# Kernel tuning notes

Measured on AMD Instinct MI355X. Metric: run time of the kernel, lower is better.

## Reference

```python
import jax, jax.numpy as jnp
import numpy as np

D = 384        # residual_depth
QK = 48        # D // qk_dim_div(=8)
E = 768        # D * expand_factor(=2)
NB = 8         # num_blocks
VOCAB = 100
LN_EPS = 1e-5


def _ln(x, g, b):
    m = x.mean(-1, keepdims=True)
    v = x.var(-1, keepdims=True)  # biased, matches torch LayerNorm
    return (x - m) / jnp.sqrt(v + LN_EPS) * g + b


def setup_inputs() -> dict:
    key = jax.random.key(0)
    ks = jax.random.split(key, 5)
    B, S = 4, 2048
    q = jax.random.randint(ks[0], (B, S), 0, 100, dtype=jnp.int32)
    freqs = jnp.exp(jnp.arange(0, D, 2, dtype=jnp.float32) * (-np.log(10000.0) / D))
    # fused expand: rows = qk + qk + expand + expand = 1632
    exp_w = (0.5 / np.sqrt(D) / 2.0) * jax.random.normal(ks[1], (NB, 2 * QK + 2 * E, D), dtype=jnp.float32)
    proj_w = (1.0 / np.sqrt(D) / 2.0 / NB) * jax.random.normal(ks[2], (NB, D, E), dtype=jnp.float32)
    blk_g = jnp.ones((NB, D), jnp.float32)
    blk_b = jnp.zeros((NB, D), jnp.float32)
    ln_g = jnp.ones((D,), jnp.float32)
    ln_b = jnp.zeros((D,), jnp.float32)
    out_w = 0.02 * jax.random.normal(ks[3], (VOCAB, D), dtype=jnp.float32)
    return dict(q=q, freqs=freqs, exp_w=exp_w, proj_w=proj_w,
                blk_g=blk_g, blk_b=blk_b, ln_g=ln_g, ln_b=ln_b, out_w=out_w)


def reference(q, freqs, exp_w, proj_w, blk_g, blk_b, ln_g, ln_b, out_w):
    S = q.shape[1]
    # sinusoidal encoding of integer tokens -> [B,S,D]
    qe = q.astype(jnp.float32)[..., None] * freqs
    x = jnp.concatenate([jnp.sin(qe), jnp.cos(qe)], axis=-1)
    x = _ln(x, ln_g, ln_b)
    # causal mask; position_bias_base is zeros in the source
    bias = jnp.where(jnp.tril(jnp.ones((S, S), bool)), 0.0, -jnp.inf).astype(jnp.float32)
    inv_sqrt_qk = 1.0 / np.sqrt(QK)

    def block(x, p):
        ew, pw, g, b = p
        xn = _ln(x, g, b)
        h = xn @ ew.T                                   # [B,S,1632]
        qh, kh, lin, pg = jnp.split(h, [QK, 2 * QK, 2 * QK + E], axis=-1)
        geglu = lin * jax.nn.gelu(pg, approximate=False)  # [B,S,E]
        loc, val = geglu[..., :E - D], geglu[..., E - D:]  # [B,S,D],[B,S,D]
        sc = jnp.einsum('bqd,bkd->bqk', qh, kh) * inv_sqrt_qk + bias
        attn = jax.nn.softmax(sc, axis=-1) @ val          # [B,S,D]
        out = jnp.concatenate([loc, attn], axis=-1) @ pw.T
        return x + out, None

    x, _ = jax.lax.scan(block, x, (exp_w, proj_w, blk_g, blk_b))
    x = _ln(x, ln_g, ln_b)
    return x @ out_w.T
```

## Files before the change

### kernel.cpp

```cpp
#include <hip/hip_runtime.h>
#include <hip/hip_bf16.h>

#define TOK 8192
#define DM 384
#define QKD 48
#define EM 768
#define NBLK 8
#define NVOCAB 100
#define SEQ 2048
#define HN 1664
#define HNV 1632
#define CH 8
#define NUNITS 2304

using short4v = __attribute__((ext_vector_type(4))) short;
using short8 = __attribute__((ext_vector_type(8))) short;
using f32x4  = __attribute__((ext_vector_type(4))) float;

static __device__ __forceinline__ float bf2f(short s) {
    union { unsigned u; float f; } c; c.u = ((unsigned)(unsigned short)s) << 16; return c.f;
}
static __device__ __forceinline__ short f2bf(float f) {
    union { float f; unsigned u; } c; c.f = f;
    unsigned r = (c.u + 0x7FFFu + ((c.u >> 16) & 1u)) >> 16;
    return (short)r;
}
static __device__ __forceinline__ void gload_lds16(const short* g, short* l) {
    __builtin_amdgcn_global_load_lds((const __attribute__((address_space(1))) void*)g,
                                     (__attribute__((address_space(3))) void*)l, 16, 0, 0);
}

__global__ void k_cvt_all(const float* __restrict__ expw, const float* __restrict__ projw,
                          const float* __restrict__ outw, short* __restrict__ ewb,
                          short* __restrict__ pwb, short* __restrict__ owb) {
    const int n1 = NBLK * HN * DM;
    for (int i = blockIdx.x * 256 + threadIdx.x; i < n1; i += gridDim.x * 256) {
        int L = i / (HN * DM); int rem = i % (HN * DM);
        int r = rem / DM; int c = rem % DM;
        float v = (r < HNV) ? expw[((size_t)L * HNV + r) * DM + c] : 0.f;
        ewb[i] = f2bf(v);
    }
    const int n2 = NBLK * DM * EM;
    for (int i = blockIdx.x * 256 + threadIdx.x; i < n2; i += gridDim.x * 256)
        pwb[i] = f2bf(projw[i]);
    const int n3 = 128 * DM;
    for (int i = blockIdx.x * 256 + threadIdx.x; i < n3; i += gridDim.x * 256) {
        int r = i / DM, c = i % DM;
        owb[i] = f2bf(r < NVOCAB ? outw[r * DM + c] : 0.f);
    }
}

__global__ __launch_bounds__(256) void k_embed(const int* __restrict__ q,
        const float* __restrict__ freqs, const float* __restrict__ lng,
        const float* __restrict__ lnb, float* __restrict__ x) {
    int wid = blockIdx.x * 4 + (threadIdx.x >> 6);
    int lane = threadIdx.x & 63;
    if (wid >= TOK) return;
    float qv = (float)q[wid];
    float v[6]; float s = 0.f, s2 = 0.f;
    #pragma unroll
    for (int i = 0; i < 6; ++i) {
        int d = lane + 64 * i;
        float val;
        if (d < 192) val = sinf(qv * freqs[d]);
        else         val = cosf(qv * freqs[d - 192]);
        v[i] = val; s += val; s2 += val * val;
    }
    #pragma unroll
    for (int m = 1; m < 64; m <<= 1) { s += __shfl_xor(s, m); s2 += __shfl_xor(s2, m); }
    float mean = s * (1.f / DM);
    float var = s2 * (1.f / DM) - mean * mean;
    float rstd = rsqrtf(var + 1e-5f);
    float* xr = x + (size_t)wid * DM;
    #pragma unroll
    for (int i = 0; i < 6; ++i) {
        int d = lane + 64 * i;
        xr[d] = (v[i] - mean) * rstd * lng[d] + lnb[d];
    }
}

__global__ __launch_bounds__(256) void k_ln(const float* __restrict__ x,
        const float* __restrict__ g, const float* __restrict__ b,
        short* __restrict__ xn) {
    int wid = blockIdx.x * 4 + (threadIdx.x >> 6);
    int lane = threadIdx.x & 63;
    if (wid >= TOK) return;
    const float* xr = x + (size_t)wid * DM;
    float v[6]; float s = 0.f, s2 = 0.f;
    #pragma unroll
    for (int i = 0; i < 6; ++i) {
        v[i] = xr[lane + 64 * i]; s += v[i]; s2 += v[i] * v[i];
    }
    #pragma unroll
    for (int m = 1; m < 64; m <<= 1) { s += __shfl_xor(s, m); s2 += __shfl_xor(s2, m); }
    float mean = s * (1.f / DM);
    float var = s2 * (1.f / DM) - mean * mean;
    float rstd = rsqrtf(var + 1e-5f);
    short* xo = xn + (size_t)wid * DM;
    #pragma unroll
    for (int i = 0; i < 6; ++i) {
        int d = lane + 64 * i;
        xo[d] = f2bf((v[i] - mean) * rstd * g[d] + b[d]);
    }
}

__global__ __launch_bounds__(256) void k_gemmh(const short* __restrict__ A,
        const short* __restrict__ Bw, short* __restrict__ cat,
        short* __restrict__ vT, short* __restrict__ qhb, short* __restrict__ khb) {
    __shared__ __align__(16) short As[128 * 32];
    __shared__ __align__(16) short Bs[128 * 32];
    int m0 = blockIdx.x * 128;
    int y = blockIdx.y;
    int t = threadIdx.x;
    int wid = t >> 6, lane = t & 63;
    int wm = (wid >> 1) * 64, wn = (wid & 1) * 64;
    int lr = lane & 15, lg = lane >> 4;
    int seg0 = wid * 2, seg1 = wid * 2 + 1;
    int row0 = seg0 * 16 + (lane >> 2), row1 = seg1 * 16 + (lane >> 2);
    int cu0 = (lane & 3) ^ ((row0 + (row0 >> 2)) & 3);
    int cu1 = (lane & 3) ^ ((row1 + (row1 >> 2)) & 3);
    int brow0, brow1;
    if (y < 12) {
        int s0h = row0 >> 4, s1h = row1 >> 4;
        brow0 = 96 + (s0h & 1) * 768 + y * 64 + (s0h >> 1) * 16 + (row0 & 15);
        brow1 = 96 + (s1h & 1) * 768 + y * 64 + (s1h >> 1) * 16 + (row1 & 15);
    } else {
        brow0 = (row0 < 96) ? row0 : 1632 + (row0 - 96);
        brow1 = (row1 < 96) ? row1 : 1632 + (row1 - 96);
    }
    const short* srcA0 = A + (size_t)(m0 + row0) * DM + cu0 * 8;
    const short* srcA1 = A + (size_t)(m0 + row1) * DM + cu1 * 8;
    const short* srcB0 = Bw + (size_t)brow0 * DM + cu0 * 8;
    const short* srcB1 = Bw + (size_t)brow1 * DM + cu1 * 8;
    short* dA0 = As + seg0 * 512; short* dA1 = As + seg1 * 512;
    short* dB0 = Bs + seg0 * 512; short* dB1 = Bs + seg1 * 512;
    const f32x4 vz = {0.f, 0.f, 0.f, 0.f};
    f32x4 acc[4][4];
    #pragma unroll
    for (int i = 0; i < 4; ++i)
        #pragma unroll
        for (int j = 0; j < 4; ++j) acc[i][j] = vz;
    for (int k0 = 0; k0 < DM; k0 += 32) {
        if (k0) __syncthreads();
        gload_lds16(srcA0 + k0, dA0);
        gload_lds16(srcA1 + k0, dA1);
        gload_lds16(srcB0 + k0, dB0);
        gload_lds16(srcB1 + k0, dB1);
        __syncthreads();
        short8 af[4], bfr[4];
        #pragma unroll
        for (int i = 0; i < 4; ++i) {
            int ra = wm + i * 16 + lr;
            int rb = wn + i * 16 + lr;
            af[i]  = *(const short8*)(As + ra * 32 + ((lg ^ ((ra + (ra >> 2)) & 3)) * 8));
            bfr[i] = *(const short8*)(Bs + rb * 32 + ((lg ^ ((rb + (rb >> 2)) & 3)) * 8));
        }
        #pragma unroll
        for (int i = 0; i < 4; ++i)
            #pragma unroll
            for (int j = 0; j < 4; ++j)
                acc[i][j] = __builtin_amdgcn_mfma_f32_16x16x32_bf16(af[i], bfr[j], acc[i][j], 0, 0, 0);
    }
    if (y < 12) {
        #pragma unroll
        for (int i = 0; i < 4; ++i) {
            int tok0 = m0 + wm + i * 16 + lg * 4;
            #pragma unroll
            for (int k = 0; k < 2; ++k) {
                int e = y * 64 + (wn >> 1) + k * 16 + lr;
                short vb[4];
                #pragma unroll
                for (int r = 0; r < 4; ++r) {
                    float l = acc[i][2 * k][r], pg = acc[i][2 * k + 1][r];
                    float gel = pg * 0.5f * (1.f + erff(pg * 0.70710678118654752f));
                    vb[r] = f2bf(l * gel);
                }
                if (y < 6) {
                    #pragma unroll
                    for (int r = 0; r < 4; ++r)
                        cat[(size_t)(tok0 + r) * EM + e] = vb[r];
                } else {
                    short4v pk = {vb[0], vb[1], vb[2], vb[3]};
                    *(short4v*)(vT + (size_t)(e - DM) * TOK + tok0) = pk;
                }
            }
        }
    } else {
        #pragma unroll
        for (int i = 0; i < 4; ++i)
            #pragma unroll
            for (int j = 0; j < 4; ++j) {
                int col = wn + j * 16 + lr;
                #pragma unroll
                for (int r = 0; r < 4; ++r) {
                    int tok = m0 + wm + i * 16 + lg * 4 + r;
                    short v = f2bf(acc[i][j][r]);
                    if (col < 64) qhb[(size_t)tok * 64 + col] = (col < QKD) ? v : (short)0;
                    if (col >= QKD && col < QKD + 64)
                        khb[(size_t)tok * 64 + col - QKD] = (col < 96) ? v : (short)0;
                }
            }
    }
}

template<int MODE>
__global__ __launch_bounds__(256) void k_gemm(const short* __restrict__ A,
        const short* __restrict__ Bw, int K, int lda, int ldb,
        void* __restrict__ Cp, int ldc) {
    __shared__ __align__(16) short As[128 * 32];
    __shared__ __align__(16) short Bs[128 * 32];
    int m0 = blockIdx.x * 128, n0 = blockIdx.y * 128;
    int t = threadIdx.x;
    int wid = t >> 6, lane = t & 63;
    int wm = (wid >> 1) * 64, wn = (wid & 1) * 64;
    int lr = lane & 15, lg = lane >> 4;
    int seg0 = wid * 2, seg1 = wid * 2 + 1;
    int row0 = seg0 * 16 + (lane >> 2), row1 = seg1 * 16 + (lane >> 2);
    int cu0 = (lane & 3) ^ ((row0 + (row0 >> 2)) & 3);
    int cu1 = (lane & 3) ^ ((row1 + (row1 >> 2)) & 3);
    const short* srcA0 = A + (size_t)(m0 + row0) * lda + cu0 * 8;
    const short* srcA1 = A + (size_t)(m0 + row1) * lda + cu1 * 8;
    const short* srcB0 = Bw + (size_t)(n0 + row0) * ldb + cu0 * 8;
    const short* srcB1 = Bw + (size_t)(n0 + row1) * ldb + cu1 * 8;
    short* dA0 = As + seg0 * 512; short* dA1 = As + seg1 * 512;
    short* dB0 = Bs + seg0 * 512; short* dB1 = Bs + seg1 * 512;
    const f32x4 vz = {0.f, 0.f, 0.f, 0.f};
    f32x4 acc[4][4];
    #pragma unroll
    for (int i = 0; i < 4; ++i)
        #pragma unroll
        for (int j = 0; j < 4; ++j) acc[i][j] = vz;
    for (int k0 = 0; k0 < K; k0 += 32) {
        if (k0) __syncthreads();
        gload_lds16(srcA0 + k0, dA0);
        gload_lds16(srcA1 + k0, dA1);
        gload_lds16(srcB0 + k0, dB0);
        gload_lds16(srcB1 + k0, dB1);
        __syncthreads();
        short8 af[4], bfr[4];
        #pragma unroll
        for (int i = 0; i < 4; ++i) {
            int ra = wm + i * 16 + lr;
            int rb = wn + i * 16 + lr;
            af[i]  = *(const short8*)(As + ra * 32 + ((lg ^ ((ra + (ra >> 2)) & 3)) * 8));
            bfr[i] = *(const short8*)(Bs + rb * 32 + ((lg ^ ((rb + (rb >> 2)) & 3)) * 8));
        }
        #pragma unroll
        for (int i = 0; i < 4; ++i)
            #pragma unroll
            for (int j = 0; j < 4; ++j)
                acc[i][j] = __builtin_amdgcn_mfma_f32_16x16x32_bf16(af[i], bfr[j], acc[i][j], 0, 0, 0);
    }
    int rb = m0 + wm + (lane >> 4) * 4;
    int cb = n0 + wn + lr;
    #pragma unroll
    for (int i = 0; i < 4; ++i)
        #pragma unroll
        for (int j = 0; j < 4; ++j)
            #pragma unroll
            for (int r = 0; r < 4; ++r) {
                int row = rb + i * 16 + r;
                int col = cb + j * 16;
                float v = acc[i][j][r];
                if (MODE == 0) ((short*)Cp)[(size_t)row * ldc + col] = f2bf(v);
                else if (MODE == 1) ((float*)Cp)[(size_t)row * ldc + col] += v;
                else if (col < NVOCAB) ((float*)Cp)[(size_t)row * NVOCAB + col] = v;
            }
}

__global__ __launch_bounds__(128) void k_gemm64(const short* __restrict__ A,
        const short* __restrict__ Bw, float* __restrict__ C) {
    __shared__ __align__(16) short As[64 * 32];
    __shared__ __align__(16) short Bs[128 * 32];
    int m0 = blockIdx.x * 64, n0 = blockIdx.y * 128;
    int t = threadIdx.x;
    int wid = t >> 6, lane = t & 63;
    int wn = wid * 64;
    int lr = lane & 15, lg = lane >> 4;
    int rsub = lane >> 2;
    int rowA0 = (wid * 2) * 16 + rsub,     rowA1 = (wid * 2 + 1) * 16 + rsub;
    int rowB0 = (wid * 4) * 16 + rsub,     rowB1 = (wid * 4 + 1) * 16 + rsub;
    int rowB2 = (wid * 4 + 2) * 16 + rsub, rowB3 = (wid * 4 + 3) * 16 + rsub;
    int q4 = lane & 3;
    int cA0 = q4 ^ ((rowA0 + (rowA0 >> 2)) & 3), cA1 = q4 ^ ((rowA1 + (rowA1 >> 2)) & 3);
    int cB0 = q4 ^ ((rowB0 + (rowB0 >> 2)) & 3), cB1 = q4 ^ ((rowB1 + (rowB1 >> 2)) & 3);
    int cB2 = q4 ^ ((rowB2 + (rowB2 >> 2)) & 3), cB3 = q4 ^ ((rowB3 + (rowB3 >> 2)) & 3);
    const short* sA0 = A + (size_t)(m0 + rowA0) * EM + cA0 * 8;
    const short* sA1 = A + (size_t)(m0 + rowA1) * EM + cA1 * 8;
    const short* sB0 = Bw + (size_t)(n0 + rowB0) * EM + cB0 * 8;
    const short* sB1 = Bw + (size_t)(n0 + rowB1) * EM + cB1 * 8;
    const short* sB2 = Bw + (size_t)(n0 + rowB2) * EM + cB2 * 8;
    const short* sB3 = Bw + (size_t)(n0 + rowB3) * EM + cB3 * 8;
    short* dA0 = As + (wid * 2) * 512;     short* dA1 = As + (wid * 2 + 1) * 512;
    short* dB0 = Bs + (wid * 4) * 512;     short* dB1 = Bs + (wid * 4 + 1) * 512;
    short* dB2 = Bs + (wid * 4 + 2) * 512; short* dB3 = Bs + (wid * 4 + 3) * 512;
    const f32x4 vz = {0.f, 0.f, 0.f, 0.f};
    f32x4 acc[4][4];
    #pragma unroll
    for (int i = 0; i < 4; ++i)
        #pragma unroll
        for (int j = 0; j < 4; ++j) acc[i][j] = vz;
    for (int k0 = 0; k0 < EM; k0 += 32) {
        if (k0) __syncthreads();
        gload_lds16(sA0 + k0, dA0);
        gload_lds16(sA1 + k0, dA1);
        gload_lds16(sB0 + k0, dB0);
        gload_lds16(sB1 + k0, dB1);
        gload_lds16(sB2 + k0, dB2);
        gload_lds16(sB3 + k0, dB3);
        __syncthreads();
        short8 af[4], bfr[4];
        #pragma unroll
        for (int i = 0; i < 4; ++i) {
            int ra = i * 16 + lr;
            int rbw = wn + i * 16 + lr;
            af[i]  = *(const short8*)(As + ra * 32 + ((lg ^ ((ra + (ra >> 2)) & 3)) * 8));
            bfr[i] = *(const short8*)(Bs + rbw * 32 + ((lg ^ ((rbw + (rbw >> 2)) & 3)) * 8));
        }
        #pragma unroll
        for (int i = 0; i < 4; ++i)
            #pragma unroll
            for (int j = 0; j < 4; ++j)
                acc[i][j] = __builtin_amdgcn_mfma_f32_16x16x32_bf16(af[i], bfr[j], acc[i][j], 0, 0, 0);
    }
    int rbase = m0 + (lane >> 4) * 4;
    int cbase = n0 + wn + lr;
    #pragma unroll
    for (int i = 0; i < 4; ++i)
        #pragma unroll
        for (int j = 0; j < 4; ++j)
            #pragma unroll
            for (int r = 0; r < 4; ++r)
                C[(size_t)(rbase + i * 16 + r) * DM + cbase + j * 16] += acc[i][j][r];
}

__global__ __launch_bounds__(256) void k_flash(const short* __restrict__ qhb,
        const short* __restrict__ khb, const short* __restrict__ vT,
        short* __restrict__ Po, float* __restrict__ Pml) {
    int idx = blockIdx.x;
    int xcd = idx & 7;
    int b = xcd >> 1;
    int unit = ((idx >> 3) << 1) | (xcd & 1);
    int gq = unit & 31, c = unit >> 5;
    if (c > (gq >> 2)) return;
    __shared__ __align__(16) short Vlds[384 * 40];
    __shared__ __align__(16) short Klds[32 * 64];
    __shared__ __align__(16) short Plds[4 * 16 * 40];
    int t = threadIdx.x;
    int wid = t >> 6, lane = t & 63;
    int lr = lane & 15, lg = lane >> 4;
    int qt = gq * 4 + wid;
    int g = qt >> 4;
    int tb = b * SEQ;
    int q0 = qt * 16;
    int nkbm = 2 * gq + 2;
    int kb0 = c * CH;
    int kb1 = min(kb0 + CH, nkbm);
    short* P = Plds + wid * (16 * 40);
    const float scale = 0.14433756729740643f;
    const float CFIX = 8.f;
    const f32x4 vzero = {0.f, 0.f, 0.f, 0.f};

    short8 qf[2];
    #pragma unroll
    for (int ks = 0; ks < 2; ++ks)
        qf[ks] = *(const short8*)(qhb + (size_t)(tb + q0 + lr) * 64 + ks * 32 + lg * 8);

    f32x4 o[24];
    #pragma unroll
    for (int j = 0; j < 24; ++j) o[j] = vzero;
    float li[4];
    #pragma unroll
    for (int r = 0; r < 4; ++r) li[r] = 0.f;

    int vrow = t >> 2, vc = (t & 3) * 8;
    const short* vsrc0 = vT + (size_t)vrow * TOK + tb + vc;
    int krow = t >> 3, kc8 = (t & 7) * 8;
    const short* ksrc0 = khb + (size_t)(tb + krow) * 64 + kc8;

    short8 rv[6], rk;
    #pragma unroll
    for (int i = 0; i < 6; ++i)
        rv[i] = *(const short8*)(vsrc0 + (size_t)(i * 64) * TOK + kb0 * 32);
    rk = *(const short8*)(ksrc0 + (size_t)kb0 * 2048);

    for (int kb = kb0; kb < kb1; ++kb) {
        int kbase = kb * 32;
        __syncthreads();
        #pragma unroll
        for (int i = 0; i < 6; ++i)
            *(short8*)(Vlds + (vrow + i * 64) * 40 + vc) = rv[i];
        *(short8*)(Klds + krow * 64 + kc8) = rk;
        if (kb + 1 < kb1) {
            #pragma unroll
            for (int i = 0; i < 6; ++i)
                rv[i] = *(const short8*)(vsrc0 + (size_t)(i * 64) * TOK + kbase + 32);
            rk = *(const short8*)(ksrc0 + (size_t)(kb + 1) * 2048);
        }
        __syncthreads();
        short8 kf0a = *(const short8*)(Klds + lr * 64 + lg * 8);
        short8 kf0b = *(const short8*)(Klds + lr * 64 + 32 + lg * 8);
        short8 kf1a = *(const short8*)(Klds + (16 + lr) * 64 + lg * 8);
        short8 kf1b = *(const short8*)(Klds + (16 + lr) * 64 + 32 + lg * 8);

        f32x4 s0 = vzero, s1 = vzero;
        s0 = __builtin_amdgcn_mfma_f32_16x16x32_bf16(qf[0], kf0a, s0, 0, 0, 0);
        s0 = __builtin_amdgcn_mfma_f32_16x16x32_bf16(qf[1], kf0b, s0, 0, 0, 0);
        s1 = __builtin_amdgcn_mfma_f32_16x16x32_bf16(qf[0], kf1a, s1, 0, 0, 0);
        s1 = __builtin_amdgcn_mfma_f32_16x16x32_bf16(qf[1], kf1b, s1, 0, 0, 0);

        bool needmask = (kbase + 31 > q0);
        #pragma unroll
        for (int r = 0; r < 4; ++r) {
            float v0 = s0[r] * scale, v1 = s1[r] * scale;
            if (needmask) {
                int qg = q0 + lg * 4 + r;
                if (kbase + lr > qg) v0 = -1e30f;
                if (kbase + 16 + lr > qg) v1 = -1e30f;
            }
            float p0 = __expf(v0 - CFIX);
            float p1 = __expf(v1 - CFIX);
            li[r] += p0 + p1;
            s0[r] = p0; s1[r] = p1;
        }
        #pragma unroll
        for (int r = 0; r < 4; ++r) {
            P[(lg * 4 + r) * 40 + lr] = f2bf(s0[r]);
            P[(lg * 4 + r) * 40 + 16 + lr] = f2bf(s1[r]);
        }
        short8 pf = *(const short8*)(P + lr * 40 + lg * 8);
        #pragma unroll
        for (int j = 0; j < 24; ++j) {
            short8 vf = *(const short8*)(Vlds + (j * 16 + lr) * 40 + lg * 8);
            o[j] = __builtin_amdgcn_mfma_f32_16x16x32_bf16(pf, vf, o[j], 0, 0, 0);
        }
    }
    #pragma unroll
    for (int r = 0; r < 4; ++r) {
        float sum = li[r];
        #pragma unroll
        for (int d2 = 1; d2 < 16; d2 <<= 1) sum += __shfl_xor(sum, d2);
        li[r] = sum;
    }
    int uid = 8 * g * (g + 1) + (qt & 15) * (g + 1) + c;
    int sidx = (uid << 2) | b;
    size_t ob = (size_t)sidx * (16 * 384);
    #pragma unroll
    for (int j = 0; j < 24; ++j)
        #pragma unroll
        for (int r = 0; r < 4; ++r)
            Po[ob + (size_t)(lg * 4 + r) * 384 + j * 16 + lr] = f2bf(o[j][r]);
    if (lr == 0) {
        #pragma unroll
        for (int r = 0; r < 4; ++r) {
            Pml[sidx * 32 + lg * 4 + r]      = CFIX;
            Pml[sidx * 32 + 16 + lg * 4 + r] = li[r];
        }
    }
}

__global__ __launch_bounds__(256) void k_comb(const short* __restrict__ Po,
        const float* __restrict__ Pml, short* __restrict__ cat) {
    int bid = blockIdx.x;
    int b = bid & 3, qt = bid >> 2;
    int g = qt >> 4;
    int nch = g + 1;
    int ubase = 8 * g * (g + 1) + (qt & 15) * (g + 1);
    int tid = threadIdx.x;
    int row = tid >> 4;
    int c0 = (tid & 15) * 24;
    float m[8], l[8], w[8];
    float M = -1e30f;
    #pragma unroll
    for (int c = 0; c < 8; ++c) {
        if (c < nch) {
            int uu = ((ubase + c) << 2) | b;
            m[c] = Pml[uu * 32 + row];
            l[c] = Pml[uu * 32 + 16 + row];
            M = fmaxf(M, m[c]);
        } else { m[c] = -1e30f; l[c] = 0.f; }
    }
    float L = 0.f;
    #pragma unroll
    for (int c = 0; c < 8; ++c) { w[c] = __expf(m[c] - M); L += l[c] * w[c]; }
    float invL = 1.f / L;
    float acc[24];
    #pragma unroll
    for (int e = 0; e < 24; ++e) acc[e] = 0.f;
    #pragma unroll
    for (int c = 0; c < 8; ++c) {
        if (c < nch) {
            int uu = ((ubase + c) << 2) | b;
            const short8* pp = (const short8*)(Po + ((size_t)uu * 16 + row) * 384 + c0);
            #pragma unroll
            for (int v = 0; v < 3; ++v) {
                short8 tv = pp[v];
                #pragma unroll
                for (int k = 0; k < 8; ++k) acc[v * 8 + k] += w[c] * bf2f(tv[k]);
            }
        }
    }
    size_t tok = (size_t)b * SEQ + qt * 16 + row;
    #pragma unroll
    for (int e = 0; e < 24; ++e)
        cat[tok * EM + DM + c0 + e] = f2bf(acc[e] * invL);
}

extern "C" void kernel_launch(void* const* d_in, const int* in_sizes, int n_in,
                              void* d_out, int out_size, void* d_ws, size_t ws_size,
                              hipStream_t stream) {
    const int*   q     = (const int*)d_in[0];
    const float* freqs = (const float*)d_in[1];
    const float* expw  = (const float*)d_in[2];
    const float* projw = (const float*)d_in[3];
    const float* blkg  = (const float*)d_in[4];
    const float* blkb  = (const float*)d_in[5];
    const float* lng   = (const float*)d_in[6];
    const float* lnb   = (const float*)d_in[7];
    const float* outw  = (const float*)d_in[8];
    float* out = (float*)d_out;

    char* p = (char*)d_ws;
    auto alloc = [&](size_t bytes) {
        char* r = p; p += (bytes + 255) & ~(size_t)255; return r;
    };
    float* x   = (float*)alloc((size_t)TOK * DM * 4);
    short* xn  = (short*)alloc((size_t)TOK * DM * 2);
    short* h   = (short*)alloc((size_t)TOK * HN * 2);
    short* cat = (short*)alloc((size_t)TOK * EM * 2);
    short* vT  = (short*)alloc((size_t)DM * TOK * 2);
    short* qhb = (short*)alloc((size_t)TOK * 64 * 2);
    short* khb = (short*)alloc((size_t)TOK * 64 * 2);
    short* ewb = (short*)alloc((size_t)NBLK * HN * DM * 2);
    short* pwb = (short*)alloc((size_t)NBLK * DM * EM * 2);
    short* owb = (short*)alloc((size_t)128 * DM * 2);
    (void)h;
    short* Po  = xn;
    float* Pml = (float*)(Po + (size_t)NUNITS * 16 * 384);

    k_cvt_all<<<2048, 256, 0, stream>>>(expw, projw, outw, ewb, pwb, owb);
    k_embed<<<TOK / 4, 256, 0, stream>>>(q, freqs, lng, lnb, x);

    for (int L = 0; L < NBLK; ++L) {
        k_ln<<<TOK / 4, 256, 0, stream>>>(x, blkg + L * DM, blkb + L * DM, xn);
        k_gemmh<<<dim3(64, 13), 256, 0, stream>>>(xn, ewb + (size_t)L * HN * DM,
                                                  cat, vT, qhb, khb);
        k_flash<<<1024, 256, 0, stream>>>(qhb, khb, vT, Po, Pml);
        k_comb<<<512, 256, 0, stream>>>(Po, Pml, cat);
        k_gemm64<<<dim3(128, 3), 128, 0, stream>>>(cat, pwb + (size_t)L * DM * EM, x);
    }
    k_ln<<<TOK / 4, 256, 0, stream>>>(x, lng, lnb, xn);
    k_gemm<2><<<dim3(64, 1), 256, 0, stream>>>(xn, owb, DM, DM, DM, out, NVOCAB);
}
```

Before: 847.2 us.

## Fuse setup kernels, deepen gemmh K-tile, and simplify flash-split combine

The weight-conversion, embedding and first block LayerNorm are merged into one setup kernel, which removes two launches and one pass over the activations. The expand GEMM now stages 64-wide K tiles with an 8-way XOR swizzle, halving the number of barrier round trips. The combine kernel drops per-chunk max rescaling because flash partials use a fixed max constant, and it writes its output with vectorized stores. The combine change depends on the flash kernel using a shared fixed max, which risks overflow if scores exceed that bound.

New measurement: 804.2 us. 1.05x faster.

```diff
diff --git a/kernel.cpp b/kernel.cpp
--- a/kernel.cpp
+++ b/kernel.cpp
@@ -30,9 +30,13 @@
                                      (__attribute__((address_space(3))) void*)l, 16, 0, 0);
 }
 
-__global__ void k_cvt_all(const float* __restrict__ expw, const float* __restrict__ projw,
-                          const float* __restrict__ outw, short* __restrict__ ewb,
-                          short* __restrict__ pwb, short* __restrict__ owb) {
+__global__ __launch_bounds__(256) void k_setup(const float* __restrict__ expw,
+        const float* __restrict__ projw, const float* __restrict__ outw,
+        short* __restrict__ ewb, short* __restrict__ pwb, short* __restrict__ owb,
+        const int* __restrict__ q, const float* __restrict__ freqs,
+        const float* __restrict__ lng, const float* __restrict__ lnb,
+        const float* __restrict__ bg0, const float* __restrict__ bb0,
+        float* __restrict__ x, short* __restrict__ xn) {
     const int n1 = NBLK * HN * DM;
     for (int i = blockIdx.x * 256 + threadIdx.x; i < n1; i += gridDim.x * 256) {
         int L = i / (HN * DM); int rem = i % (HN * DM);
@@ -48,14 +52,8 @@
         int r = i / DM, c = i % DM;
         owb[i] = f2bf(r < NVOCAB ? outw[r * DM + c] : 0.f);
     }
-}
-
-__global__ __launch_bounds__(256) void k_embed(const int* __restrict__ q,
-        const float* __restrict__ freqs, const float* __restrict__ lng,
-        const float* __restrict__ lnb, float* __restrict__ x) {
     int wid = blockIdx.x * 4 + (threadIdx.x >> 6);
     int lane = threadIdx.x & 63;
-    if (wid >= TOK) return;
     float qv = (float)q[wid];
     float v[6]; float s = 0.f, s2 = 0.f;
     #pragma unroll
@@ -72,10 +70,24 @@
     float var = s2 * (1.f / DM) - mean * mean;
     float rstd = rsqrtf(var + 1e-5f);
     float* xr = x + (size_t)wid * DM;
+    float s3 = 0.f, s4 = 0.f;
     #pragma unroll
     for (int i = 0; i < 6; ++i) {
         int d = lane + 64 * i;
-        xr[d] = (v[i] - mean) * rstd * lng[d] + lnb[d];
+        v[i] = (v[i] - mean) * rstd * lng[d] + lnb[d];
+        xr[d] = v[i];
+        s3 += v[i]; s4 += v[i] * v[i];
+    }
+    #pragma unroll
+    for (int m = 1; m < 64; m <<= 1) { s3 += __shfl_xor(s3, m); s4 += __shfl_xor(s4, m); }
+    float mean2 = s3 * (1.f / DM);
+    float var2 = s4 * (1.f / DM) - mean2 * mean2;
+    float rstd2 = rsqrtf(var2 + 1e-5f);
+    short* xo = xn + (size_t)wid * DM;
+    #pragma unroll
+    for (int i = 0; i < 6; ++i) {
+        int d = lane + 64 * i;
+        xo[d] = f2bf((v[i] - mean2) * rstd2 * bg0[d] + bb0[d]);
     }
 }
 
@@ -107,59 +119,62 @@
 __global__ __launch_bounds__(256) void k_gemmh(const short* __restrict__ A,
         const short* __restrict__ Bw, short* __restrict__ cat,
         short* __restrict__ vT, short* __restrict__ qhb, short* __restrict__ khb) {
-    __shared__ __align__(16) short As[128 * 32];
-    __shared__ __align__(16) short Bs[128 * 32];
+    __shared__ __align__(16) short As[128 * 64];
+    __shared__ __align__(16) short Bs[128 * 64];
     int m0 = blockIdx.x * 128;
     int y = blockIdx.y;
     int t = threadIdx.x;
     int wid = t >> 6, lane = t & 63;
     int wm = (wid >> 1) * 64, wn = (wid & 1) * 64;
     int lr = lane & 15, lg = lane >> 4;
-    int seg0 = wid * 2, seg1 = wid * 2 + 1;
-    int row0 = seg0 * 16 + (lane >> 2), row1 = seg1 * 16 + (lane >> 2);
-    int cu0 = (lane & 3) ^ ((row0 + (row0 >> 2)) & 3);
-    int cu1 = (lane & 3) ^ ((row1 + (row1 >> 2)) & 3);
-    int brow0, brow1;
-    if (y < 12) {
-        int s0h = row0 >> 4, s1h = row1 >> 4;
-        brow0 = 96 + (s0h & 1) * 768 + y * 64 + (s0h >> 1) * 16 + (row0 & 15);
-        brow1 = 96 + (s1h & 1) * 768 + y * 64 + (s1h >> 1) * 16 + (row1 & 15);
-    } else {
-        brow0 = (row0 < 96) ? row0 : 1632 + (row0 - 96);
-        brow1 = (row1 < 96) ? row1 : 1632 + (row1 - 96);
-    }
-    const short* srcA0 = A + (size_t)(m0 + row0) * DM + cu0 * 8;
-    const short* srcA1 = A + (size_t)(m0 + row1) * DM + cu1 * 8;
-    const short* srcB0 = Bw + (size_t)brow0 * DM + cu0 * 8;
-    const short* srcB1 = Bw + (size_t)brow1 * DM + cu1 * 8;
-    short* dA0 = As + seg0 * 512; short* dA1 = As + seg1 * 512;
-    short* dB0 = Bs + seg0 * 512; short* dB1 = Bs + seg1 * 512;
+    int srow = wid * 32 + (lane >> 3);
+    int sck = (lane & 7) ^ (lane >> 3);
+    auto bmap = [&](int row) {
+        if (y < 12) {
+            int sh = row >> 4;
+            return 96 + (sh & 1) * 768 + y * 64 + (sh >> 1) * 16 + (row & 15);
+        }
+        return (row < 96) ? row : 1632 + (row - 96);
+    };
+    const short* srcA[4]; const short* srcB[4]; short* dstA[4]; short* dstB[4];
+    #pragma unroll
+    for (int i = 0; i < 4; ++i) {
+        int row = srow + i * 8;
+        srcA[i] = A + (size_t)(m0 + row) * DM + sck * 8;
+        srcB[i] = Bw + (size_t)bmap(row) * DM + sck * 8;
+        dstA[i] = As + wid * 2048 + i * 512;
+        dstB[i] = Bs + wid * 2048 + i * 512;
+    }
     const f32x4 vz = {0.f, 0.f, 0.f, 0.f};
     f32x4 acc[4][4];
     #pragma unroll
     for (int i = 0; i < 4; ++i)
         #pragma unroll
         for (int j = 0; j < 4; ++j) acc[i][j] = vz;
-    for (int k0 = 0; k0 < DM; k0 += 32) {
+    for (int k0 = 0; k0 < DM; k0 += 64) {
         if (k0) __syncthreads();
-        gload_lds16(srcA0 + k0, dA0);
-        gload_lds16(srcA1 + k0, dA1);
-        gload_lds16(srcB0 + k0, dB0);
-        gload_lds16(srcB1 + k0, dB1);
+        #pragma unroll
+        for (int i = 0; i < 4; ++i) {
+            gload_lds16(srcA[i] + k0, dstA[i]);
+            gload_lds16(srcB[i] + k0, dstB[i]);
+        }
         __syncthreads();
-        short8 af[4], bfr[4];
-        #pragma unroll
-        for (int i = 0; i < 4; ++i) {
-            int ra = wm + i * 16 + lr;
-            int rb = wn + i * 16 + lr;
-            af[i]  = *(const short8*)(As + ra * 32 + ((lg ^ ((ra + (ra >> 2)) & 3)) * 8));
-            bfr[i] = *(const short8*)(Bs + rb * 32 + ((lg ^ ((rb + (rb >> 2)) & 3)) * 8));
-        }
-        #pragma unroll
-        for (int i = 0; i < 4; ++i)
-            #pragma unroll
-            for (int j = 0; j < 4; ++j)
-                acc[i][j] = __builtin_amdgcn_mfma_f32_16x16x32_bf16(af[i], bfr[j], acc[i][j], 0, 0, 0);
+        #pragma unroll
+        for (int ks = 0; ks < 2; ++ks) {
+            short8 af[4], bfr[4];
+            #pragma unroll
+            for (int i = 0; i < 4; ++i) {
+                int ra = wm + i * 16 + lr;
+                int rb = wn + i * 16 + lr;
+                af[i]  = *(const short8*)(As + ra * 64 + (((lg + ks * 4) ^ (ra & 7)) * 8));
+                bfr[i] = *(const short8*)(Bs + rb * 64 + (((lg + ks * 4) ^ (rb & 7)) * 8));
+            }
+            #pragma unroll
+            for (int i = 0; i < 4; ++i)
+                #pragma unroll
+                for (int j = 0; j < 4; ++j)
+                    acc[i][j] = __builtin_amdgcn_mfma_f32_16x16x32_bf16(af[i], bfr[j], acc[i][j], 0, 0, 0);
+        }
     }
     if (y < 12) {
         #pragma unroll
@@ -452,10 +467,8 @@
             Po[ob + (size_t)(lg * 4 + r) * 384 + j * 16 + lr] = f2bf(o[j][r]);
     if (lr == 0) {
         #pragma unroll
-        for (int r = 0; r < 4; ++r) {
-            Pml[sidx * 32 + lg * 4 + r]      = CFIX;
+        for (int r = 0; r < 4; ++r)
             Pml[sidx * 32 + 16 + lg * 4 + r] = li[r];
-        }
     }
 }
 
@@ -469,41 +482,34 @@
     int tid = threadIdx.x;
     int row = tid >> 4;
     int c0 = (tid & 15) * 24;
-    float m[8], l[8], w[8];
-    float M = -1e30f;
+    float L = 0.f;
+    float acc[24];
+    #pragma unroll
+    for (int e = 0; e < 24; ++e) acc[e] = 0.f;
     #pragma unroll
     for (int c = 0; c < 8; ++c) {
         if (c < nch) {
             int uu = ((ubase + c) << 2) | b;
-            m[c] = Pml[uu * 32 + row];
-            l[c] = Pml[uu * 32 + 16 + row];
-            M = fmaxf(M, m[c]);
-        } else { m[c] = -1e30f; l[c] = 0.f; }
-    }
-    float L = 0.f;
-    #pragma unroll
-    for (int c = 0; c < 8; ++c) { w[c] = __expf(m[c] - M); L += l[c] * w[c]; }
-    float invL = 1.f / L;
-    float acc[24];
-    #pragma unroll
-    for (int e = 0; e < 24; ++e) acc[e] = 0.f;
-    #pragma unroll
-    for (int c = 0; c < 8; ++c) {
-        if (c < nch) {
-            int uu = ((ubase + c) << 2) | b;
+            L += Pml[uu * 32 + 16 + row];
             const short8* pp = (const short8*)(Po + ((size_t)uu * 16 + row) * 384 + c0);
             #pragma unroll
             for (int v = 0; v < 3; ++v) {
                 short8 tv = pp[v];
                 #pragma unroll
-                for (int k = 0; k < 8; ++k) acc[v * 8 + k] += w[c] * bf2f(tv[k]);
+                for (int k = 0; k < 8; ++k) acc[v * 8 + k] += bf2f(tv[k]);
             }
         }
     }
+    float invL = 1.f / L;
     size_t tok = (size_t)b * SEQ + qt * 16 + row;
-    #pragma unroll
-    for (int e = 0; e < 24; ++e)
-        cat[tok * EM + DM + c0 + e] = f2bf(acc[e] * invL);
+    short* dst = cat + tok * EM + DM + c0;
+    #pragma unroll
+    for (int v = 0; v < 3; ++v) {
+        short8 o8;
+        #pragma unroll
+        for (int k = 0; k < 8; ++k) o8[k] = f2bf(acc[v * 8 + k] * invL);
+        *(short8*)(dst + v * 8) = o8;
+    }
 }
 
 extern "C" void kernel_launch(void* const* d_in, const int* in_sizes, int n_in,
@@ -538,11 +544,11 @@
     short* Po  = xn;
     float* Pml = (float*)(Po + (size_t)NUNITS * 16 * 384);
 
-    k_cvt_all<<<2048, 256, 0, stream>>>(expw, projw, outw, ewb, pwb, owb);
-    k_embed<<<TOK / 4, 256, 0, stream>>>(q, freqs, lng, lnb, x);
+    k_setup<<<2048, 256, 0, stream>>>(expw, projw, outw, ewb, pwb, owb,
+                                      q, freqs, lng, lnb, blkg, blkb, x, xn);
 
     for (int L = 0; L < NBLK; ++L) {
-        k_ln<<<TOK / 4, 256, 0, stream>>>(x, blkg + L * DM, blkb + L * DM, xn);
+        if (L) k_ln<<<TOK / 4, 256, 0, stream>>>(x, blkg + L * DM, blkb + L * DM, xn);
         k_gemmh<<<dim3(64, 13), 256, 0, stream>>>(xn, ewb + (size_t)L * HN * DM,
                                                   cat, vT, qhb, khb);
         k_flash<<<1024, 256, 0, stream>>>(qhb, khb, vT, Po, Pml);
```
